# Kernel optimization log

Measured on AMD Instinct MI355X. Metric: run time of the kernel, lower is better.

Reference implementation:

```python
import jax, jax.numpy as jnp
import numpy as np

T, XDIM, ZDIM = 500000, 64, 64


def setup_inputs() -> dict:
    key = jax.random.key(0)
    ks = jax.random.split(key, 6)
    return {
        "X_t": jax.random.normal(ks[0], (T, XDIM), dtype=jnp.float32),
        "Z_t": jax.random.normal(ks[1], (T, ZDIM), dtype=jnp.float32),
        "G": jax.random.uniform(ks[2], (), dtype=jnp.float32),
        "eta": jax.random.normal(ks[3], (XDIM,), dtype=jnp.float32),
        "zeta": jax.random.normal(ks[4], (ZDIM,), dtype=jnp.float32),
        "gamma": jax.random.normal(ks[5], (ZDIM,), dtype=jnp.float32),
    }


def reference(X_t, Z_t, G, eta, zeta, gamma):
    # theta_t = sigmoid(G) * theta_{t-1} + dot(Z[t-1], gamma), theta_0 = 0
    # Y_t = theta_t + dot(X[t], eta) + dot(Z[t], zeta)
    G_hat = jax.nn.sigmoid(G)  # addSigmoid=True path
    c = Z_t @ gamma                                   # [T]
    u = jnp.concatenate([jnp.zeros((1,), c.dtype), c[:-1]])  # shifted drive, u_0 = 0
    a = jnp.full_like(u, G_hat)

    def combine(x, y):
        a1, b1 = x
        a2, b2 = y
        return a1 * a2, b1 * a2 + b2

    _, theta = jax.lax.associative_scan(combine, (a, u))  # [T], theta_0 = 0
    return theta + X_t @ eta + Z_t @ zeta
```

## Files before the change

kernel.cpp:

```cpp
#include <hip/hip_runtime.h>


#define WIN    64
#define CHUNK  1024
#define SEG    4
#define RPI    64
#define NITER  ((WIN + CHUNK) / RPI)

__global__ __launch_bounds__(256) void dlm_fused(
    const float* __restrict__ X, const float* __restrict__ Z,
    const float* __restrict__ Gp,
    const float* __restrict__ eta, const float* __restrict__ zeta,
    const float* __restrict__ gam,
    float* __restrict__ out, int T)
{
    const int tid  = threadIdx.x;
    const int lane = tid & 63;
    const int wv   = tid >> 6;
    const int sub  = lane & 15;
    const int rsub = lane >> 4;
    const int s    = (int)blockIdx.x * CHUNK;

    __shared__ float cl[WIN + CHUNK];
    __shared__ float bl[CHUNK];
    __shared__ float sc[256];
    __shared__ float theta_sh;

    const float4 e4  = ((const float4*)eta)[sub];
    const float4 sz4 = ((const float4*)zeta)[sub];
    const float4 g4  = ((const float4*)gam)[sub];
    const float4* X4 = (const float4*)X;
    const float4* Z4 = (const float4*)Z;

    const float g   = *Gp;
    const float a   = 1.0f / (1.0f + expf(-g));
    const float l2a = log2f(a);

    for (int i = 0; i < NITER; ++i) {
        const int rb = s - WIN + i * RPI + wv * 16;
        float cp[4], bp[4];
        #pragma unroll
        for (int u = 0; u < 4; ++u) {
            const int r = rb + u * 4 + rsub;
            float4 z = make_float4(0.f, 0.f, 0.f, 0.f);
            float4 x = make_float4(0.f, 0.f, 0.f, 0.f);
            const bool in = (r >= 0) && (r < T);
            if (in)           z = Z4[(size_t)r * 16 + sub];
            if (in && i > 0)  x = X4[(size_t)r * 16 + sub];
            cp[u] = z.x*g4.x + z.y*g4.y + z.z*g4.z + z.w*g4.w;
            bp[u] = x.x*e4.x + x.y*e4.y + x.z*e4.z + x.w*e4.w
                  + z.x*sz4.x + z.y*sz4.y + z.z*sz4.z + z.w*sz4.w;
        }
        #pragma unroll
        for (int u = 0; u < 4; ++u) {
            #pragma unroll
            for (int off = 1; off <= 8; off <<= 1) {
                cp[u] += __shfl_xor(cp[u], off, 64);
                bp[u] += __shfl_xor(bp[u], off, 64);
            }
        }
        if (sub == 0) {
            #pragma unroll
            for (int u = 0; u < 4; ++u) {
                const int r = rb + u * 4 + rsub;
                cl[r - s + WIN] = cp[u];
                if (i > 0) bl[r - s] = bp[u];
            }
        }
    }
    __syncthreads();

    if (tid < 64) {
        float term = 0.0f;
        if (tid <= WIN - 2)
            term = exp2f((float)tid * l2a) * cl[WIN - 2 - tid];
        #pragma unroll
        for (int off = 1; off <= 32; off <<= 1)
            term += __shfl_xor(term, off, 64);
        if (tid == 0) theta_sh = term;
    }

    const float a2 = a * a, A4 = a2 * a2;
    const int p0 = tid * SEG;
    float sl = 0.0f;
    #pragma unroll
    for (int j = 0; j < SEG; ++j) {
        const int t = s + p0 + j;
        const float v = (t == 0) ? 0.0f : cl[WIN + p0 + j - 1];
        sl = a * sl + v;
    }
    sc[tid] = sl;
    __syncthreads();
    const float theta_in = theta_sh;

    float Ad = A4;
    for (int d = 1; d < 256; d <<= 1) {
        const float self = sc[tid];
        const float prev = (tid >= d) ? sc[tid - d] : 0.0f;
        __syncthreads();
        sc[tid] = self + Ad * prev;
        __syncthreads();
        Ad *= Ad;
    }

    const float E = (tid > 0) ? sc[tid - 1] : 0.0f;
    float theta = exp2f((float)(SEG * tid) * l2a) * theta_in + E;
    float res[SEG];
    #pragma unroll
    for (int j = 0; j < SEG; ++j) {
        const int t = s + p0 + j;
        const float v = (t == 0) ? 0.0f : cl[WIN + p0 + j - 1];
        theta = a * theta + v;
        res[j] = bl[p0 + j] + theta;
    }
    const int t0 = s + p0;
    if (t0 + SEG <= T) {
        ((float4*)out)[(s >> 2) + tid] = make_float4(res[0], res[1], res[2], res[3]);
    } else {
        #pragma unroll
        for (int j = 0; j < SEG; ++j)
            if (t0 + j < T) out[t0 + j] = res[j];
    }
}

extern "C" void kernel_launch(void* const* d_in, const int* in_sizes, int n_in,
                              void* d_out, int out_size, void* d_ws, size_t ws_size,
                              hipStream_t stream) {
    const float* X     = (const float*)d_in[0];
    const float* Z     = (const float*)d_in[1];
    const float* G     = (const float*)d_in[2];
    const float* eta   = (const float*)d_in[3];
    const float* zeta  = (const float*)d_in[4];
    const float* gamma = (const float*)d_in[5];
    float* out = (float*)d_out;

    const int T = in_sizes[0] / 64;
    const int nblk = (T + CHUNK - 1) / CHUNK;

    dlm_fused<<<nblk, 256, 0, stream>>>(X, Z, G, eta, zeta, gamma, out, T);
}
```

Measured before the change: 278.6 us.

## Assign one row per thread with smaller chunks and flat block scan

```diff
diff --git a/kernel.cpp b/kernel.cpp
--- a/kernel.cpp
+++ b/kernel.cpp
@@ -1,73 +1,59 @@
 #include <hip/hip_runtime.h>
 
 
-#define WIN    64
-#define CHUNK  1024
-#define SEG    4
-#define RPI    64
-#define NITER  ((WIN + CHUNK) / RPI)
+#define WIN   64
+#define CHUNK 256
+#define NTHR  (WIN + CHUNK)
 
-__global__ __launch_bounds__(256) void dlm_fused(
+__global__ __launch_bounds__(NTHR, 8) void dlm_fused(
     const float* __restrict__ X, const float* __restrict__ Z,
     const float* __restrict__ Gp,
     const float* __restrict__ eta, const float* __restrict__ zeta,
     const float* __restrict__ gam,
     float* __restrict__ out, int T)
 {
-    const int tid  = threadIdx.x;
-    const int lane = tid & 63;
-    const int wv   = tid >> 6;
-    const int sub  = lane & 15;
-    const int rsub = lane >> 4;
-    const int s    = (int)blockIdx.x * CHUNK;
+    const int tid = threadIdx.x;
+    const int s   = (int)blockIdx.x * CHUNK;
+    const int r   = s - WIN + tid;
 
-    __shared__ float cl[WIN + CHUNK];
+    __shared__ float cl[NTHR];
     __shared__ float bl[CHUNK];
-    __shared__ float sc[256];
+    __shared__ float sc[CHUNK];
     __shared__ float theta_sh;
-
-    const float4 e4  = ((const float4*)eta)[sub];
-    const float4 sz4 = ((const float4*)zeta)[sub];
-    const float4 g4  = ((const float4*)gam)[sub];
-    const float4* X4 = (const float4*)X;
-    const float4* Z4 = (const float4*)Z;
 
     const float g   = *Gp;
     const float a   = 1.0f / (1.0f + expf(-g));
     const float l2a = log2f(a);
 
-    for (int i = 0; i < NITER; ++i) {
-        const int rb = s - WIN + i * RPI + wv * 16;
-        float cp[4], bp[4];
+    const bool rowok = (r >= 0) && (r < T);
+
+    float c = 0.0f, b = 0.0f;
+    if (rowok) {
+        const float4* Zr = (const float4*)Z + (size_t)r * 16;
+        const float4* G4 = (const float4*)gam;
+        const float4* S4 = (const float4*)zeta;
         #pragma unroll
-        for (int u = 0; u < 4; ++u) {
-            const int r = rb + u * 4 + rsub;
-            float4 z = make_float4(0.f, 0.f, 0.f, 0.f);
-            float4 x = make_float4(0.f, 0.f, 0.f, 0.f);
-            const bool in = (r >= 0) && (r < T);
-            if (in)           z = Z4[(size_t)r * 16 + sub];
-            if (in && i > 0)  x = X4[(size_t)r * 16 + sub];
-            cp[u] = z.x*g4.x + z.y*g4.y + z.z*g4.z + z.w*g4.w;
-            bp[u] = x.x*e4.x + x.y*e4.y + x.z*e4.z + x.w*e4.w
-                  + z.x*sz4.x + z.y*sz4.y + z.z*sz4.z + z.w*sz4.w;
-        }
-        #pragma unroll
-        for (int u = 0; u < 4; ++u) {
-            #pragma unroll
-            for (int off = 1; off <= 8; off <<= 1) {
-                cp[u] += __shfl_xor(cp[u], off, 64);
-                bp[u] += __shfl_xor(bp[u], off, 64);
-            }
-        }
-        if (sub == 0) {
-            #pragma unroll
-            for (int u = 0; u < 4; ++u) {
-                const int r = rb + u * 4 + rsub;
-                cl[r - s + WIN] = cp[u];
-                if (i > 0) bl[r - s] = bp[u];
-            }
+        for (int j = 0; j < 16; ++j) {
+            float4 z = Zr[j];
+            float4 gv = G4[j];
+            float4 sv = S4[j];
+            c += z.x*gv.x + z.y*gv.y + z.z*gv.z + z.w*gv.w;
+            b += z.x*sv.x + z.y*sv.y + z.z*sv.z + z.w*sv.w;
         }
     }
+    if (rowok && tid >= WIN) {
+        const float4* Xr = (const float4*)X + (size_t)r * 16;
+        const float4* E4 = (const float4*)eta;
+        #pragma unroll
+        for (int j = 0; j < 16; ++j) {
+            float4 x = Xr[j];
+            float4 ev = E4[j];
+            b += x.x*ev.x + x.y*ev.y + x.z*ev.z + x.w*ev.w;
+        }
+    }
+
+    cl[tid] = rowok ? c : 0.0f;
+    if (tid >= WIN) bl[tid - WIN] = b;
     __syncthreads();
 
     if (tid < 64) {
@@ -80,46 +66,27 @@
         if (tid == 0) theta_sh = term;
     }
 
-    const float a2 = a * a, A4 = a2 * a2;
-    const int p0 = tid * SEG;
-    float sl = 0.0f;
-    #pragma unroll
-    for (int j = 0; j < SEG; ++j) {
-        const int t = s + p0 + j;
-        const float v = (t == 0) ? 0.0f : cl[WIN + p0 + j - 1];
-        sl = a * sl + v;
-    }
-    sc[tid] = sl;
+    if (tid < CHUNK)
+        sc[tid] = (s + tid == 0) ? 0.0f : cl[WIN + tid - 1];
     __syncthreads();
-    const float theta_in = theta_sh;
 
-    float Ad = A4;
-    for (int d = 1; d < 256; d <<= 1) {
-        const float self = sc[tid];
-        const float prev = (tid >= d) ? sc[tid - d] : 0.0f;
+    float Ad = a;
+    for (int d = 1; d < CHUNK; d <<= 1) {
+        float self = 0.0f, prev = 0.0f;
+        if (tid < CHUNK) {
+            self = sc[tid];
+            prev = (tid >= d) ? sc[tid - d] : 0.0f;
+        }
         __syncthreads();
-        sc[tid] = self + Ad * prev;
+        if (tid < CHUNK) sc[tid] = self + Ad * prev;
         __syncthreads();
         Ad *= Ad;
     }
 
-    const float E = (tid > 0) ? sc[tid - 1] : 0.0f;
-    float theta = exp2f((float)(SEG * tid) * l2a) * theta_in + E;
-    float res[SEG];
-    #pragma unroll
-    for (int j = 0; j < SEG; ++j) {
-        const int t = s + p0 + j;
-        const float v = (t == 0) ? 0.0f : cl[WIN + p0 + j - 1];
-        theta = a * theta + v;
-        res[j] = bl[p0 + j] + theta;
-    }
-    const int t0 = s + p0;
-    if (t0 + SEG <= T) {
-        ((float4*)out)[(s >> 2) + tid] = make_float4(res[0], res[1], res[2], res[3]);
-    } else {
-        #pragma unroll
-        for (int j = 0; j < SEG; ++j)
-            if (t0 + j < T) out[t0 + j] = res[j];
+    const int t = s + tid;
+    if (tid < CHUNK && t < T) {
+        float theta = exp2f((float)(tid + 1) * l2a) * theta_sh + sc[tid];
+        out[t] = bl[tid] + theta;
     }
 }
 
@@ -137,5 +104,5 @@
     const int T = in_sizes[0] / 64;
     const int nblk = (T + CHUNK - 1) / CHUNK;
 
-    dlm_fused<<<nblk, 256, 0, stream>>>(X, Z, G, eta, zeta, gamma, out, T);
+    dlm_fused<<<nblk, NTHR, 0, stream>>>(X, Z, G, eta, zeta, gamma, out, T);
 }
```

After: 291.5 us. 1.05x slower.

## Double-buffer X/Z tiles into LDS via async global_load_lds and halve chunk size

Applied to the files above, without the earlier changes.

```diff
diff --git a/kernel.cpp b/kernel.cpp
--- a/kernel.cpp
+++ b/kernel.cpp
@@ -2,12 +2,19 @@
 
 
 #define WIN    64
-#define CHUNK  1024
-#define SEG    4
-#define RPI    64
-#define NITER  ((WIN + CHUNK) / RPI)
+#define CHUNK  512
+#define NTHR   256
+#define TR     32
+#define NT     ((WIN + CHUNK) / TR)
+#define SEG    2
 
-__global__ __launch_bounds__(256) void dlm_fused(
+__device__ __forceinline__ void ld_lds_1kb(const float* g, float* l) {
+    __builtin_amdgcn_global_load_lds(
+        (const __attribute__((address_space(1))) void*)g,
+        (__attribute__((address_space(3))) void*)l, 16, 0, 0);
+}
+
+__global__ __launch_bounds__(NTHR) void dlm_fused(
     const float* __restrict__ X, const float* __restrict__ Z,
     const float* __restrict__ Gp,
     const float* __restrict__ eta, const float* __restrict__ zeta,
@@ -21,54 +28,70 @@
     const int rsub = lane >> 4;
     const int s    = (int)blockIdx.x * CHUNK;
 
+    __shared__ float zb[2][TR * 64];
+    __shared__ float xb[2][TR * 64];
     __shared__ float cl[WIN + CHUNK];
     __shared__ float bl[CHUNK];
-    __shared__ float sc[256];
+    __shared__ float sc[NTHR];
     __shared__ float theta_sh;
 
-    const float4 e4  = ((const float4*)eta)[sub];
-    const float4 sz4 = ((const float4*)zeta)[sub];
-    const float4 g4  = ((const float4*)gam)[sub];
-    const float4* X4 = (const float4*)X;
-    const float4* Z4 = (const float4*)Z;
+    const float4 e4 = ((const float4*)eta)[sub];
+    const float4 z4c = ((const float4*)zeta)[sub];
+    const float4 g4 = ((const float4*)gam)[sub];
 
     const float g   = *Gp;
     const float a   = 1.0f / (1.0f + expf(-g));
     const float l2a = log2f(a);
 
-    for (int i = 0; i < NITER; ++i) {
-        const int rb = s - WIN + i * RPI + wv * 16;
-        float cp[4], bp[4];
+    auto stage = [&](int t, int b) {
         #pragma unroll
-        for (int u = 0; u < 4; ++u) {
-            const int r = rb + u * 4 + rsub;
-            float4 z = make_float4(0.f, 0.f, 0.f, 0.f);
-            float4 x = make_float4(0.f, 0.f, 0.f, 0.f);
-            const bool in = (r >= 0) && (r < T);
-            if (in)           z = Z4[(size_t)r * 16 + sub];
-            if (in && i > 0)  x = X4[(size_t)r * 16 + sub];
-            cp[u] = z.x*g4.x + z.y*g4.y + z.z*g4.z + z.w*g4.w;
-            bp[u] = x.x*e4.x + x.y*e4.y + x.z*e4.z + x.w*e4.w
-                  + z.x*sz4.x + z.y*sz4.y + z.z*sz4.z + z.w*sz4.w;
+        for (int q = 0; q < 2; ++q) {
+            const int lr = wv * 8 + q * 4;
+            const int g0 = s - WIN + t * TR + lr;
+            float* zdst = &zb[b][lr * 64];
+            const bool ok = (g0 >= 0) && (g0 + 4 <= T);
+            if (ok) ld_lds_1kb(Z + (size_t)g0 * 64 + lane * 4, zdst);
+            else    ((float4*)zdst)[lane] = make_float4(0.f, 0.f, 0.f, 0.f);
+            if (t >= 2) {
+                float* xdst = &xb[b][lr * 64];
+                if (ok) ld_lds_1kb(X + (size_t)g0 * 64 + lane * 4, xdst);
+                else    ((float4*)xdst)[lane] = make_float4(0.f, 0.f, 0.f, 0.f);
+            }
         }
+    };
+
+    auto compute = [&](int t, int b) {
         #pragma unroll
-        for (int u = 0; u < 4; ++u) {
+        for (int rg = 0; rg < 2; ++rg) {
+            const int lr  = wv * 8 + rg * 4 + rsub;
+            const int rel = t * TR + lr;
+            float4 z = ((const float4*)&zb[b][lr * 64])[sub];
+            float c  = z.x*g4.x + z.y*g4.y + z.z*g4.z + z.w*g4.w;
+            float bs = z.x*z4c.x + z.y*z4c.y + z.z*z4c.z + z.w*z4c.w;
+            if (t >= 2) {
+                float4 x = ((const float4*)&xb[b][lr * 64])[sub];
+                bs += x.x*e4.x + x.y*e4.y + x.z*e4.z + x.w*e4.w;
+            }
             #pragma unroll
             for (int off = 1; off <= 8; off <<= 1) {
-                cp[u] += __shfl_xor(cp[u], off, 64);
-                bp[u] += __shfl_xor(bp[u], off, 64);
+                c  += __shfl_xor(c,  off, 64);
+                bs += __shfl_xor(bs, off, 64);
+            }
+            if (sub == 0) {
+                cl[rel] = c;
+                if (t >= 2) bl[rel - WIN] = bs;
             }
         }
-        if (sub == 0) {
-            #pragma unroll
-            for (int u = 0; u < 4; ++u) {
-                const int r = rb + u * 4 + rsub;
-                cl[r - s + WIN] = cp[u];
-                if (i > 0) bl[r - s] = bp[u];
-            }
-        }
+    };
+
+    stage(0, 0);
+    stage(1, 1);
+    for (int t = 0; t < NT; ++t) {
+        __syncthreads();
+        compute(t, t & 1);
+        __syncthreads();
+        if (t + 2 < NT) stage(t + 2, t & 1);
     }
-    __syncthreads();
 
     if (tid < 64) {
         float term = 0.0f;
@@ -80,7 +103,7 @@
         if (tid == 0) theta_sh = term;
     }
 
-    const float a2 = a * a, A4 = a2 * a2;
+    const float A2 = a * a;
     const int p0 = tid * SEG;
     float sl = 0.0f;
     #pragma unroll
@@ -93,8 +116,8 @@
     __syncthreads();
     const float theta_in = theta_sh;
 
-    float Ad = A4;
-    for (int d = 1; d < 256; d <<= 1) {
+    float Ad = A2;
+    for (int d = 1; d < NTHR; d <<= 1) {
         const float self = sc[tid];
         const float prev = (tid >= d) ? sc[tid - d] : 0.0f;
         __syncthreads();
@@ -115,7 +138,7 @@
     }
     const int t0 = s + p0;
     if (t0 + SEG <= T) {
-        ((float4*)out)[(s >> 2) + tid] = make_float4(res[0], res[1], res[2], res[3]);
+        ((float2*)out)[(s >> 1) + tid] = make_float2(res[0], res[1]);
     } else {
         #pragma unroll
         for (int j = 0; j < SEG; ++j)
@@ -137,5 +160,5 @@
     const int T = in_sizes[0] / 64;
     const int nblk = (T + CHUNK - 1) / CHUNK;
 
-    dlm_fused<<<nblk, 256, 0, stream>>>(X, Z, G, eta, zeta, gamma, out, T);
+    dlm_fused<<<nblk, NTHR, 0, stream>>>(X, Z, G, eta, zeta, gamma, out, T);
 }
```

Measured after the change: 282.0 us. No clear change (+1.2%).
